# Kernel tuning notes

Hardware: AMD Instinct MI355X
Metric: run time of the kernel (lower is better)

## Reference

```python
import jax, jax.numpy as jnp
import numpy as np
from jax import lax


def _conv(x, w, b, pad, dil):
    # standard NCHW conv, OIHW weights
    y = lax.conv_general_dilated(x, w, (1, 1), [(pad, pad), (pad, pad)],
                                 rhs_dilation=(dil, dil),
                                 dimension_numbers=('NCHW', 'OIHW', 'NCHW'))
    return y + b[None, :, None, None]


def _bilinear(img, py, px):
    # img: [B,C,H,W]; py,px: [B,KK,H,W] float sample positions.
    # Zero-padding bilinear sampling (torchvision deform_conv semantics):
    # each of the 4 corners contributes 0 if it lies outside the image.
    B, C, H, W = img.shape
    y0 = jnp.floor(py)
    x0 = jnp.floor(px)
    wy1 = py - y0
    wx1 = px - x0
    imgf = img.reshape(B, C, H * W)

    def corner(yi, xi, wgt):
        valid = (yi >= 0) & (yi <= H - 1) & (xi >= 0) & (xi <= W - 1)
        yc = jnp.clip(yi, 0, H - 1).astype(jnp.int32)
        xc = jnp.clip(xi, 0, W - 1).astype(jnp.int32)
        idx = yc * W + xc  # [B,KK,H,W]
        g = jax.vmap(lambda im, ix: jnp.take(im, ix.reshape(-1), axis=1))(imgf, idx)
        g = g.reshape(B, C, *yi.shape[1:])  # [B,C,KK,H,W]
        return g * (wgt * valid.astype(img.dtype))[:, None]

    return (corner(y0, x0, (1 - wy1) * (1 - wx1))
            + corner(y0, x0 + 1, (1 - wy1) * wx1)
            + corner(y0 + 1, x0, wy1 * (1 - wx1))
            + corner(y0 + 1, x0 + 1, wy1 * wx1))


def _deform_dw(x, off_w, off_b, dw_w, K, pad, dil):
    # offset-predicted deformable depthwise conv (groups == channels)
    B, C, H, W = x.shape
    off = _conv(x, off_w, off_b, pad, dil).reshape(B, K * K, 2, H, W)
    dy, dx = off[:, :, 0], off[:, :, 1]  # torchvision order: (dy, dx) per tap
    ky, kx = jnp.meshgrid(jnp.arange(K), jnp.arange(K), indexing='ij')
    by = (ky.reshape(-1) * dil - pad).astype(x.dtype)  # [KK]
    bx = (kx.reshape(-1) * dil - pad).astype(x.dtype)
    py = jnp.arange(H, dtype=x.dtype)[None, None, :, None] + by[None, :, None, None] + dy
    px = jnp.arange(W, dtype=x.dtype)[None, None, None, :] + bx[None, :, None, None] + dx
    s = _bilinear(x, py, px)  # [B,C,KK,H,W]
    return jnp.einsum('bckhw,ck->bchw', s, dw_w.reshape(C, K * K))


def setup_inputs() -> dict:
    key = jax.random.key(0)
    ks = jax.random.split(key, 9)
    B, C, H, W = 4, 64, 56, 56
    f = lambda k, shape, s: jax.random.normal(k, shape, jnp.float32) * s
    return dict(
        x=f(ks[0], (B, C, H, W), 1.0),
        off_w1=f(ks[1], (2 * 5 * 5, C, 5, 5), 0.01), off_b1=f(ks[2], (2 * 5 * 5,), 0.01),
        dw_w1=f(ks[3], (C, 1, 5, 5), 0.1),
        off_w2=f(ks[4], (2 * 7 * 7, C, 7, 7), 0.01), off_b2=f(ks[5], (2 * 7 * 7,), 0.01),
        dw_w2=f(ks[6], (C, 1, 7, 7), 0.1),
        pw_w=f(ks[7], (C, C, 1, 1), 0.05), pw_b=f(ks[8], (C,), 0.05),
    )


def reference(x, off_w1, off_b1, dw_w1, off_w2, off_b2, dw_w2, pw_w, pw_b):
    attn = _deform_dw(x, off_w1, off_b1, dw_w1, 5, 2, 1)       # 5x5 deformable dw
    attn = _deform_dw(attn, off_w2, off_b2, dw_w2, 7, 9, 3)    # 7x7 dil-3 deformable dw
    attn = _conv(attn, pw_w, pw_b, 0, 1)                       # 1x1 pointwise
    return x * attn                                            # gated multiply
```

## Files before the change

kernel.cpp:

```cpp
#include <hip/hip_runtime.h>

#define BB 4
#define CC 64
#define HH 56
#define WW 56
#define HW (HH*WW)

typedef unsigned short u16;
typedef unsigned int u32;
typedef __attribute__((ext_vector_type(8))) short bf16x8;
typedef __attribute__((ext_vector_type(4))) float f32x4;

__device__ __forceinline__ u16 f2bf(float f) {
    union { float f; unsigned u; } c; c.f = f;
    unsigned u = c.u;
    u = (u + 0x7FFFu + ((u >> 16) & 1u)) >> 16;
    return (u16)u;
}
__device__ __forceinline__ float lo_f(u32 u) {
    union { unsigned u; float f; } c; c.u = u << 16; return c.f;
}
__device__ __forceinline__ float hi_f(u32 u) {
    union { unsigned u; float f; } c; c.u = u & 0xffff0000u; return c.f;
}

#define R1 102400
#define R2 401408
#define R3 4096
#define R4 1600
#define R5 3136
#define TGRID (BB*(HW/64))
#define PREPN (R1+R2+R3+R4+R5)
__global__ __launch_bounds__(256)
void prep_tr_kernel(const float* __restrict__ x,
                    const float* __restrict__ ow1, const float* __restrict__ ow2,
                    const float* __restrict__ pw,  const float* __restrict__ dw1,
                    const float* __restrict__ dw2,
                    u16* __restrict__ xT,
                    u16* __restrict__ w2t1, u16* __restrict__ w2t2,
                    u16* __restrict__ pwT, float* __restrict__ dwT1,
                    float* __restrict__ dwT2) {
    __shared__ u16 tile[64][72];
    const int t = threadIdx.x;
    if (blockIdx.x < TGRID) {
        const int blk = blockIdx.x;
        const int b   = blk / (HW/64);
        const int p0  = (blk % (HW/64))*64;
        const int px  = t & 63, icq = t >> 6;
        const float* ip = x + ((size_t)b*CC + icq*16)*HW + p0 + px;
        #pragma unroll
        for (int i = 0; i < 16; ++i)
            tile[px][icq*16 + i] = f2bf(ip[(size_t)i*HW]);
        __syncthreads();
        const int px2 = t >> 2, g = t & 3;
        u16* op = xT + ((size_t)b*HW + p0 + px2)*64 + g*16;
        const uint4* s = (const uint4*)&tile[px2][g*16];
        ((uint4*)op)[0] = s[0];
        ((uint4*)op)[1] = s[1];
        return;
    }
    const int i = (blockIdx.x - TGRID)*256 + t;
    if (i < R1) {
        const int ic = i & 63, n = (i >> 6) & 63, tap = i >> 12;
        w2t1[i] = f2bf((n < 50) ? ow1[((size_t)n*64 + ic)*25 + tap] : 0.f);
    } else if (i < R1+R2) {
        const int j = i - R1;
        const int ic = j & 63, n = (j >> 6) & 127, tap = j >> 13;
        w2t2[j] = f2bf((n < 98) ? ow2[((size_t)n*64 + ic)*49 + tap] : 0.f);
    } else if (i < R1+R2+R3) {
        const int j = i - (R1+R2);
        pwT[j] = f2bf(pw[j]);
    } else if (i < R1+R2+R3+R4) {
        const int j = i - (R1+R2+R3);
        const int c = j & 63, k = j >> 6;
        dwT1[j] = dw1[c*25 + k];
    } else if (i < R1+R2+R3+R4+R5) {
        const int j = i - (R1+R2+R3+R4);
        const int c = j & 63, k = j >> 6;
        dwT2[j] = dw2[c*49 + k];
    }
}

__device__ __forceinline__ uint4 selz(bool v, uint4 a) {
    const uint4 z = make_uint4(0,0,0,0);
    return v ? a : z;
}

template<int K, int DIL, int PAD, int COUT, int NP, int NPAD, int NTW>
__global__ __launch_bounds__(256, 4)
void conv_mfma_lds_kernel(const u16* __restrict__ xT, const u16* __restrict__ w2t,
                          const float* __restrict__ bias, float* __restrict__ out) {
    constexpr int KK = K*K;
    constexpr int BROWS = 16*NTW;
    __shared__ u16 Ab[2][64*64];
    __shared__ u16 Bb[2][BROWS*64];

    const int nm   = HW/64;
    const int b    = blockIdx.x / nm;
    const int p0   = (blockIdx.x % nm)*64;
    const int nt0  = blockIdx.y;
    const int t    = threadIdx.x;
    const int wave = t >> 6;
    const int lane = t & 63;

    const int spx = t >> 3;
    const int sc  = t & 7;
    const int pA  = p0 + spx;
    const int pB  = p0 + spx + 32;
    const int pyA = pA / WW, pxA = pA % WW;
    const int pyB = pB / WW, pxB = pB % WW;
    const u16* xb = xT + (size_t)b*HW*64;
    const int sslotA = ((sc + spx) & 7)*8;
    const int bn  = t >> 3;
    const int bslot = ((sc + bn) & 7)*8;
    const u16* wbase = w2t + (size_t)nt0*BROWS*64;

    const int r = lane & 15, quad = lane >> 4;
    const int mloc = wave*16 + r;
    const int arow = mloc*64;
    const int a0s = ((quad     + mloc) & 7)*8;
    const int a1s = ((quad + 4 + mloc) & 7)*8;
    const int b0s = ((quad     + r) & 7)*8;
    const int b1s = ((quad + 4 + r) & 7)*8;

    f32x4 acc[NTW];
    #pragma unroll
    for (int h = 0; h < NTW; ++h) acc[h] = (f32x4){0.f,0.f,0.f,0.f};
    const uint4 z4 = make_uint4(0,0,0,0);

    auto LD = [&](int tap, uint4& a0, uint4& a1, bool& va, bool& vb, uint4& bb) {
        const int dyy = (tap/K)*DIL - PAD;
        const int dxx = (tap%K)*DIL - PAD;
        const int off = dyy*WW + dxx;
        {
            const int yy = pyA + dyy, xx = pxA + dxx;
            va = ((unsigned)yy < (unsigned)HH) && ((unsigned)xx < (unsigned)WW);
            a0 = *(const uint4*)(xb + (size_t)(va ? (pA + off) : 0)*64 + sc*8);
        }
        {
            const int yy = pyB + dyy, xx = pxB + dxx;
            vb = ((unsigned)yy < (unsigned)HH) && ((unsigned)xx < (unsigned)WW);
            a1 = *(const uint4*)(xb + (size_t)(vb ? (pB + off) : 0)*64 + sc*8);
        }
        if (BROWS == 32 || bn < BROWS)
            bb = *(const uint4*)(wbase + ((size_t)tap*NP + bn)*64 + sc*8);
    };

    uint4 rA0 = z4, rA1 = z4, rB = z4;
    bool v0 = false, v1 = false;
    LD(0, rA0, rA1, v0, v1, rB);

    #pragma unroll
    for (int tap = 0; tap < KK; ++tap) {
        uint4 nA0 = z4, nA1 = z4, nB = z4;
        bool nv0 = false, nv1 = false;
        if (tap + 1 < KK) LD(tap + 1, nA0, nA1, nv0, nv1, nB);

        u16* A  = &Ab[tap & 1][0];
        u16* Bq = &Bb[tap & 1][0];
        *(uint4*)(A + spx*64      + sslotA) = selz(v0, rA0);
        *(uint4*)(A + (spx+32)*64 + sslotA) = selz(v1, rA1);
        if (BROWS == 32 || bn < BROWS) *(uint4*)(Bq + bn*64 + bslot) = rB;
        __syncthreads();

        const bf16x8 av0 = *(const bf16x8*)(A + arow + a0s);
        const bf16x8 av1 = *(const bf16x8*)(A + arow + a1s);
        #pragma unroll
        for (int h = 0; h < NTW; ++h) {
            const int brow = (h*16 + r)*64;
            const bf16x8 bv0 = *(const bf16x8*)(Bq + brow + b0s);
            const bf16x8 bv1 = *(const bf16x8*)(Bq + brow + b1s);
            acc[h] = __builtin_amdgcn_mfma_f32_16x16x32_bf16(av0, bv0, acc[h], 0, 0, 0);
            acc[h] = __builtin_amdgcn_mfma_f32_16x16x32_bf16(av1, bv1, acc[h], 0, 0, 0);
        }

        rA0 = nA0; rA1 = nA1; rB = nB; v0 = nv0; v1 = nv1;
    }

    #pragma unroll
    for (int h = 0; h < NTW; ++h) {
        const int n = nt0*BROWS + h*16 + r;
        if (n < COUT) {
            const float bv = bias[n];
            float* op = out + ((size_t)b*HW + p0 + wave*16 + quad*4)*NPAD + n;
            #pragma unroll
            for (int r2 = 0; r2 < 4; ++r2) op[(size_t)r2*NPAD] = acc[h][r2] + bv;
        }
    }
}

template<int K, int DIL, int PAD, int NPAD>
__global__ __launch_bounds__(256)
void deform_cl_kernel(const u16* __restrict__ inT, const float* __restrict__ offT,
                      const float* __restrict__ dwT, u16* __restrict__ outT) {
    constexpr int KK = K*K;
    __shared__ float4 swt[8][KK];
    __shared__ int4   sat[8][KK];
    __shared__ float  sdw[KK*64];

    const int t = threadIdx.x;
    const int nb8 = (BB*HW/8) >> 3;
    const int blk0 = blockIdx.x;
    const int blk = (blk0 & 7)*nb8 + (blk0 >> 3);
    const int p0 = blk*8;
    const int b  = p0 / HW;
    const int pl0 = p0 - b*HW;

    for (int i = t; i < KK*64; i += 256) sdw[i] = dwT[i];

    for (int i = t; i < 8*KK; i += 256) {
        const int pix = i / KK, k = i - pix*KK;
        const int pl  = pl0 + pix;
        const int h = pl / WW, w = pl % WW;
        const float* orow = offT + ((size_t)b*HW + pl)*NPAD;
        const float dy = orow[2*k];
        const float dx = orow[2*k+1];
        const float py = (float)(h + (k/K)*DIL - PAD) + dy;
        const float px = (float)(w + (k%K)*DIL - PAD) + dx;
        const float y0f = floorf(py), x0f = floorf(px);
        const float wy1 = py - y0f,  wx1 = px - x0f;
        const float wy0 = 1.f - wy1, wx0 = 1.f - wx1;
        const int y0 = (int)y0f, x0 = (int)x0f;

        const int y0c = min(max(y0,   0), HH-1);
        const int y1c = min(max(y0+1, 0), HH-1);
        const int x0c = min(max(x0,   0), WW-1);
        const int x1c = min(max(x0+1, 0), WW-1);
        const float gy0 = wy0 * ((y0   >= 0 && y0   < HH) ? 1.f : 0.f);
        const float gy1 = wy1 * ((y0+1 >= 0 && y0+1 < HH) ? 1.f : 0.f);
        const float gx0 = wx0 * ((x0   >= 0 && x0   < WW) ? 1.f : 0.f);
        const float gx1 = wx1 * ((x0+1 >= 0 && x0+1 < WW) ? 1.f : 0.f);

        swt[pix][k] = make_float4(gy0*gx0, gy0*gx1, gy1*gx0, gy1*gx1);
        const int r0 = y0c*WW, r1 = y1c*WW;
        sat[pix][k] = make_int4((r0 + x0c) << 7, (r0 + x1c) << 7,
                                (r1 + x0c) << 7, (r1 + x1c) << 7);
    }
    __syncthreads();

    const int wave = t >> 6, lane = t & 63;
    const int pixl = 2*wave + (lane >> 5);
    const int chp  = lane & 31;
    const char* ib = (const char*)(inT + (size_t)b*HW*64) + chp*4;

    float accx = 0.f, accy = 0.f;

    int4   av[4];
    float4 wv[2];
    float2 dv[2];
    u32 c00[3], c01[3], c10[3], c11[3];

    av[0] = sat[pixl][0];
    if (KK > 1) av[1] = sat[pixl][1];
    if (KK > 2) av[2] = sat[pixl][2];
    wv[0] = swt[pixl][0];
    dv[0] = *(const float2*)&sdw[2*chp];
    c00[0] = *(const u32*)(ib + av[0].x);
    c01[0] = *(const u32*)(ib + av[0].y);
    c10[0] = *(const u32*)(ib + av[0].z);
    c11[0] = *(const u32*)(ib + av[0].w);
    if (KK > 1) {
        c00[1] = *(const u32*)(ib + av[1].x);
        c01[1] = *(const u32*)(ib + av[1].y);
        c10[1] = *(const u32*)(ib + av[1].z);
        c11[1] = *(const u32*)(ib + av[1].w);
    }

    #pragma unroll
    for (int k = 0; k < KK; ++k) {
        if (k + 3 < KK) av[(k+3)&3] = sat[pixl][k+3];
        if (k + 2 < KK) {
            const int4 a = av[(k+2)&3];
            c00[(k+2)%3] = *(const u32*)(ib + a.x);
            c01[(k+2)%3] = *(const u32*)(ib + a.y);
            c10[(k+2)%3] = *(const u32*)(ib + a.z);
            c11[(k+2)%3] = *(const u32*)(ib + a.w);
        }
        if (k + 1 < KK) {
            wv[(k+1)&1] = swt[pixl][k+1];
            dv[(k+1)&1] = *(const float2*)&sdw[(k+1)*64 + 2*chp];
        }
        const float4 w = wv[k&1];
        const u32 u00 = c00[k%3], u01 = c01[k%3], u10 = c10[k%3], u11 = c11[k%3];
        const float sx = lo_f(u00)*w.x + lo_f(u01)*w.y + lo_f(u10)*w.z + lo_f(u11)*w.w;
        const float sy = hi_f(u00)*w.x + hi_f(u01)*w.y + hi_f(u10)*w.z + hi_f(u11)*w.w;
        const float2 d = dv[k&1];
        accx += sx * d.x;
        accy += sy * d.y;
    }

    const u32 o = (u32)f2bf(accx) | ((u32)f2bf(accy) << 16);
    *(u32*)((char*)outT + (size_t)(p0 + pixl)*128 + chp*4) = o;
}

__global__ __launch_bounds__(256)
void pw_mfma_kernel(const u16* __restrict__ a2T, const u16* __restrict__ pwT,
                    const float* __restrict__ pb, const float* __restrict__ x,
                    float* __restrict__ out) {
    const int nm = HW/64;
    const int b  = blockIdx.x / nm;
    const int p0 = (blockIdx.x % nm)*64 + (threadIdx.x >> 6)*16;
    const int nt = blockIdx.y;
    const int lane = threadIdx.x & 63;
    const int r = lane & 15, quad = lane >> 4;

    const u16* ap = a2T + ((size_t)b*HW + p0 + r)*64 + quad*8;
    f32x4 acc = (f32x4){0.f,0.f,0.f,0.f};
    #pragma unroll
    for (int ks = 0; ks < 2; ++ks) {
        const bf16x8 av = *(const bf16x8*)(ap + ks*32);
        const bf16x8 bv = *(const bf16x8*)(pwT + ((size_t)(nt*16 + r))*64 + ks*32 + quad*8);
        acc = __builtin_amdgcn_mfma_f32_16x16x32_bf16(av, bv, acc, 0, 0, 0);
    }

    const int n = nt*16 + r;
    const float bv = pb[n];
    const size_t base = ((size_t)b*CC + n)*HW + p0 + quad*4;
    #pragma unroll
    for (int r2 = 0; r2 < 4; ++r2)
        out[base + r2] = x[base + r2] * (acc[r2] + bv);
}

template<int K, int DIL, int PAD, int COUT, int OCB>
__global__ __launch_bounds__(256)
void off_conv_sg_kernel(const float* __restrict__ in, const float* __restrict__ wgt,
                        const float* __restrict__ bias, float* __restrict__ out) {
    constexpr int KK = K*K;
    const int nOB = COUT / OCB;
    const int b   = blockIdx.x / nOB;
    const int oc0 = (blockIdx.x % nOB) * OCB;
    const int x   = threadIdx.x;
    const int h   = blockIdx.y*4 + threadIdx.y;

    float acc[OCB];
    #pragma unroll
    for (int o = 0; o < OCB; ++o) acc[o] = bias[oc0+o];

    const float* inb = in + (size_t)b*CC*HW;
    const float* wb  = wgt + (size_t)oc0*CC*KK;

    for (int ic = 0; ic < CC; ++ic) {
        const float* inp = inb + ic*HW;
        const float* wp  = wb + ic*KK;
        #pragma unroll
        for (int ky = 0; ky < K; ++ky) {
            const int  y  = h + ky*DIL - PAD;
            const bool yv = (y >= 0) && (y < HH);
            const int  yc = yv ? y : 0;
            const float* row = inp + yc*WW;
            #pragma unroll
            for (int kx = 0; kx < K; ++kx) {
                const int  xx = x + kx*DIL - PAD;
                const bool v  = yv && (xx >= 0) && (xx < WW);
                const int  xc = (xx < 0) ? 0 : ((xx >= WW) ? (WW-1) : xx);
                float val = row[xc];
                val = v ? val : 0.f;
                const int t = ky*K + kx;
                #pragma unroll
                for (int o = 0; o < OCB; ++o)
                    acc[o] += wp[(size_t)o*CC*KK + t] * val;
            }
        }
    }

    if (x >= WW) return;
    #pragma unroll
    for (int o = 0; o < OCB; ++o)
        out[((size_t)b*COUT + oc0 + o)*HW + h*WW + x] = acc[o];
}

template<int K, int DIL, int PAD>
__global__ __launch_bounds__(64)
void deform_dw_full_kernel(const float* __restrict__ in, const float* __restrict__ off,
                           const float* __restrict__ dw, float* __restrict__ out) {
    constexpr int KK = K*K;
    const int idx = blockIdx.x*64 + threadIdx.x;
    const int x = idx % WW;
    const int h = (idx / WW) % HH;
    const int c = (idx / HW) % CC;
    const int b = idx / (CC*HW);

    const float* inp  = in  + ((size_t)b*CC + c)*HW;
    const float* offp = off + (size_t)b*(2*KK)*HW + h*WW + x;
    const float* dwp  = dw  + c*KK;

    float acc = 0.f;
    #pragma unroll 7
    for (int k = 0; k < KK; ++k) {
        const float dy = offp[(2*k  )*HW];
        const float dx = offp[(2*k+1)*HW];
        const float py = (float)(h + (k/K)*DIL - PAD) + dy;
        const float px = (float)(x + (k%K)*DIL - PAD) + dx;
        const float y0f = floorf(py), x0f = floorf(px);
        const float wy1 = py - y0f,  wx1 = px - x0f;
        const float wy0 = 1.f - wy1, wx0 = 1.f - wx1;
        const int y0 = (int)y0f, x0 = (int)x0f;

        const int y0c = min(max(y0,   0), HH-1);
        const int y1c = min(max(y0+1, 0), HH-1);
        const int x0c = min(max(x0,   0), WW-1);
        const int x1c = min(max(x0+1, 0), WW-1);
        const float my0 = (y0   >= 0 && y0   < HH) ? 1.f : 0.f;
        const float my1 = (y0+1 >= 0 && y0+1 < HH) ? 1.f : 0.f;
        const float mx0 = (x0   >= 0 && x0   < WW) ? 1.f : 0.f;
        const float mx1 = (x0+1 >= 0 && x0+1 < WW) ? 1.f : 0.f;

        const float v00 = inp[y0c*WW + x0c];
        const float v01 = inp[y0c*WW + x1c];
        const float v10 = inp[y1c*WW + x0c];
        const float v11 = inp[y1c*WW + x1c];

        const float gx0 = wx0*mx0, gx1 = wx1*mx1;
        const float s = (v00*gx0 + v01*gx1) * (wy0*my0)
                      + (v10*gx0 + v11*gx1) * (wy1*my1);
        acc += s * dwp[k];
    }
    out[idx] = acc;
}

__global__ __launch_bounds__(256)
void pw_mul_kernel(const float* __restrict__ x, const float* __restrict__ a2,
                   const float* __restrict__ pw, const float* __restrict__ pb,
                   float* __restrict__ out) {
    constexpr int HW4 = HW/4;
    const int t = blockIdx.x*256 + threadIdx.x;
    if (t >= BB*CC*HW4) return;
    const int sp4 = t % HW4;
    const int oc  = (t / HW4) % CC;
    const int b   = t / (CC*HW4);

    const float4* ap = (const float4*)(a2 + (size_t)b*CC*HW) + sp4;
    const float4* wp4 = (const float4*)(pw + oc*CC);
    const float pbv = pb[oc];
    float4 acc = make_float4(pbv, pbv, pbv, pbv);
    #pragma unroll 4
    for (int ic4 = 0; ic4 < CC/4; ++ic4) {
        const float4 w = wp4[ic4];
        float4 a0 = ap[(ic4*4+0)*HW4];
        float4 a1 = ap[(ic4*4+1)*HW4];
        float4 a2v = ap[(ic4*4+2)*HW4];
        float4 a3 = ap[(ic4*4+3)*HW4];
        acc.x += w.x*a0.x + w.y*a1.x + w.z*a2v.x + w.w*a3.x;
        acc.y += w.x*a0.y + w.y*a1.y + w.z*a2v.y + w.w*a3.y;
        acc.z += w.x*a0.z + w.y*a1.z + w.z*a2v.z + w.w*a3.z;
        acc.w += w.x*a0.w + w.y*a1.w + w.z*a2v.w + w.w*a3.w;
    }
    const float4 xv = ((const float4*)x)[t];
    float4 r;
    r.x = xv.x*acc.x; r.y = xv.y*acc.y; r.z = xv.z*acc.z; r.w = xv.w*acc.w;
    ((float4*)out)[t] = r;
}

extern "C" void kernel_launch(void* const* d_in, const int* in_sizes, int n_in,
                              void* d_out, int out_size, void* d_ws, size_t ws_size,
                              hipStream_t stream) {
    const float* x      = (const float*)d_in[0];
    const float* off_w1 = (const float*)d_in[1];
    const float* off_b1 = (const float*)d_in[2];
    const float* dw_w1  = (const float*)d_in[3];
    const float* off_w2 = (const float*)d_in[4];
    const float* off_b2 = (const float*)d_in[5];
    const float* dw_w2  = (const float*)d_in[6];
    const float* pw_w   = (const float*)d_in[7];
    const float* pw_b   = (const float*)d_in[8];
    float* out = (float*)d_out;

    const size_t nF    = (size_t)BB*CC*HW;
    const size_t attnB = nF*sizeof(float);
    const size_t off2B = (size_t)BB*98*HW*sizeof(float);
    const size_t offTB = (size_t)BB*HW*112*sizeof(float);
    const size_t chB   = (size_t)BB*HW*64*sizeof(u16);
    char* ws = (char*)d_ws;

    const int n    = (int)nF;
    const int dbl  = n/64;
    const int pbl  = (n/4 + 255)/256;
    dim3 cblk(64,4);
    dim3 rgrd1(BB*(50/5), HH/4);
    dim3 rgrd2(BB*(98/7), HH/4);
    dim3 cgrd1(TGRID, 2);
    dim3 cgrd2(TGRID, 4);
    dim3 pgrd(TGRID, 4);
    const int dgrid = BB*HW/8;

    const size_t oOFF  = 0;
    const size_t oXT   = oOFF + offTB;
    const size_t oA1T  = oXT  + chB;
    const size_t oA2T  = oA1T + chB;
    const size_t oW1   = oA2T + chB;
    const size_t oW2   = oW1  + (size_t)R1*2;
    const size_t oPWT  = oW2  + (size_t)R2*2;
    const size_t oDW1  = oPWT + (size_t)R3*2;
    const size_t oDW2  = oDW1 + (size_t)R4*4;
    const size_t TOT   = oDW2 + (size_t)R5*4;

    if (ws_size >= TOT) {
        float* off_buf = (float*)(ws + oOFF);
        u16*   xT      = (u16*)(ws + oXT);
        u16*   a1T     = (u16*)(ws + oA1T);
        u16*   a2T     = (u16*)(ws + oA2T);
        u16*   w2t1    = (u16*)(ws + oW1);
        u16*   w2t2    = (u16*)(ws + oW2);
        u16*   pwT     = (u16*)(ws + oPWT);
        float* dwT1    = (float*)(ws + oDW1);
        float* dwT2    = (float*)(ws + oDW2);

        prep_tr_kernel<<<TGRID + (PREPN+255)/256, 256, 0, stream>>>(
            x, off_w1, off_w2, pw_w, dw_w1, dw_w2,
            xT, w2t1, w2t2, pwT, dwT1, dwT2);

        conv_mfma_lds_kernel<5,1,2,50,64,64,2><<<cgrd1, 256, 0, stream>>>(xT, w2t1, off_b1, off_buf);
        deform_cl_kernel<5,1,2,64><<<dgrid, 256, 0, stream>>>(xT, off_buf, dwT1, a1T);

        conv_mfma_lds_kernel<7,3,9,98,128,112,2><<<cgrd2, 256, 0, stream>>>(a1T, w2t2, off_b2, off_buf);
        deform_cl_kernel<7,3,9,112><<<dgrid, 256, 0, stream>>>(a1T, off_buf, dwT2, a2T);

        pw_mfma_kernel<<<pgrd, 256, 0, stream>>>(a2T, pwT, pw_b, x, out);
    } else if (ws_size >= off2B + attnB) {
        float* off_buf = (float*)ws;
        float* attn1   = (float*)d_out;
        float* attn2   = (float*)(ws + off2B);
        off_conv_sg_kernel<5,1,2,50,5><<<rgrd1, cblk, 0, stream>>>(x, off_w1, off_b1, off_buf);
        deform_dw_full_kernel<5,1,2><<<dbl, 64, 0, stream>>>(x, off_buf, dw_w1, attn1);
        off_conv_sg_kernel<7,3,9,98,7><<<rgrd2, cblk, 0, stream>>>(attn1, off_w2, off_b2, off_buf);
        deform_dw_full_kernel<7,3,9><<<dbl, 64, 0, stream>>>(attn1, off_buf, dw_w2, attn2);
        pw_mul_kernel<<<pbl, 256, 0, stream>>>(x, attn2, pw_w, pw_b, out);
    } else {
        float* attn1 = (float*)d_out;
        float* attn2 = (float*)ws;
        float* off1  = (float*)ws;
        off_conv_sg_kernel<5,1,2,50,5><<<rgrd1, cblk, 0, stream>>>(x, off_w1, off_b1, off1);
        deform_dw_full_kernel<5,1,2><<<dbl, 64, 0, stream>>>(x, off1, dw_w1, attn1);
        float* off2 = (float*)(ws + attnB);
        off_conv_sg_kernel<7,3,9,98,7><<<rgrd2, cblk, 0, stream>>>(attn1, off_w2, off_b2, off2);
        deform_dw_full_kernel<7,3,9><<<dbl, 64, 0, stream>>>(attn1, off2, dw_w2, attn2);
        pw_mul_kernel<<<pbl, 256, 0, stream>>>(x, attn2, pw_w, pw_b, out);
    }
}
```

Measured before the change: 155.4 us.

## Fuse second deformable depthwise stage with pointwise MFMA and gating

Merges the 7x7 deformable depthwise kernel with the 1x1 pointwise conv and gated multiply. Each block computes 8 pixels of attention, stages the bf16 result in shared memory reused from the weight table, then runs MFMA against the pointwise weights and writes x*attn directly. This removes one launch and the a2T global write and read. In exchange the MFMA is only half used (16-row tile, 8 valid pixels), and the output stores are narrow and strided across channels.

Result: no change. 153.2 us (-1.5%).

```diff
diff --git a/kernel.cpp b/kernel.cpp
--- a/kernel.cpp
+++ b/kernel.cpp
@@ -293,32 +293,130 @@
     *(u32*)((char*)outT + (size_t)(p0 + pixl)*128 + chp*4) = o;
 }
 
+template<int K, int DIL, int PAD, int NPAD>
 __global__ __launch_bounds__(256)
-void pw_mfma_kernel(const u16* __restrict__ a2T, const u16* __restrict__ pwT,
-                    const float* __restrict__ pb, const float* __restrict__ x,
-                    float* __restrict__ out) {
-    const int nm = HW/64;
-    const int b  = blockIdx.x / nm;
-    const int p0 = (blockIdx.x % nm)*64 + (threadIdx.x >> 6)*16;
-    const int nt = blockIdx.y;
-    const int lane = threadIdx.x & 63;
+void deform_pw_kernel(const u16* __restrict__ inT, const float* __restrict__ offT,
+                      const float* __restrict__ dwT, const u16* __restrict__ pwT,
+                      const float* __restrict__ pb, const float* __restrict__ x,
+                      float* __restrict__ out) {
+    constexpr int KK = K*K;
+    __shared__ float4 swt[8][KK];
+    __shared__ int4   sat[8][KK];
+    __shared__ float  sdw[KK*64];
+
+    const int t = threadIdx.x;
+    const int nb8 = (BB*HW/8) >> 3;
+    const int blk0 = blockIdx.x;
+    const int blk = (blk0 & 7)*nb8 + (blk0 >> 3);
+    const int p0 = blk*8;
+    const int b  = p0 / HW;
+    const int pl0 = p0 - b*HW;
+
+    for (int i = t; i < KK*64; i += 256) sdw[i] = dwT[i];
+
+    for (int i = t; i < 8*KK; i += 256) {
+        const int pix = i / KK, k = i - pix*KK;
+        const int pl  = pl0 + pix;
+        const int h = pl / WW, w = pl % WW;
+        const float* orow = offT + ((size_t)b*HW + pl)*NPAD;
+        const float dy = orow[2*k];
+        const float dx = orow[2*k+1];
+        const float py = (float)(h + (k/K)*DIL - PAD) + dy;
+        const float px = (float)(w + (k%K)*DIL - PAD) + dx;
+        const float y0f = floorf(py), x0f = floorf(px);
+        const float wy1 = py - y0f,  wx1 = px - x0f;
+        const float wy0 = 1.f - wy1, wx0 = 1.f - wx1;
+        const int y0 = (int)y0f, x0 = (int)x0f;
+
+        const int y0c = min(max(y0,   0), HH-1);
+        const int y1c = min(max(y0+1, 0), HH-1);
+        const int x0c = min(max(x0,   0), WW-1);
+        const int x1c = min(max(x0+1, 0), WW-1);
+        const float gy0 = wy0 * ((y0   >= 0 && y0   < HH) ? 1.f : 0.f);
+        const float gy1 = wy1 * ((y0+1 >= 0 && y0+1 < HH) ? 1.f : 0.f);
+        const float gx0 = wx0 * ((x0   >= 0 && x0   < WW) ? 1.f : 0.f);
+        const float gx1 = wx1 * ((x0+1 >= 0 && x0+1 < WW) ? 1.f : 0.f);
+
+        swt[pix][k] = make_float4(gy0*gx0, gy0*gx1, gy1*gx0, gy1*gx1);
+        const int r0 = y0c*WW, r1 = y1c*WW;
+        sat[pix][k] = make_int4((r0 + x0c) << 7, (r0 + x1c) << 7,
+                                (r1 + x0c) << 7, (r1 + x1c) << 7);
+    }
+    __syncthreads();
+
+    const int wave = t >> 6, lane = t & 63;
+    const int pixl = 2*wave + (lane >> 5);
+    const int chp  = lane & 31;
+    const char* ib = (const char*)(inT + (size_t)b*HW*64) + chp*4;
+
+    float accx = 0.f, accy = 0.f;
+
+    int4   av[4];
+    float4 wv[2];
+    float2 dv[2];
+    u32 c00[3], c01[3], c10[3], c11[3];
+
+    av[0] = sat[pixl][0];
+    if (KK > 1) av[1] = sat[pixl][1];
+    if (KK > 2) av[2] = sat[pixl][2];
+    wv[0] = swt[pixl][0];
+    dv[0] = *(const float2*)&sdw[2*chp];
+    c00[0] = *(const u32*)(ib + av[0].x);
+    c01[0] = *(const u32*)(ib + av[0].y);
+    c10[0] = *(const u32*)(ib + av[0].z);
+    c11[0] = *(const u32*)(ib + av[0].w);
+    if (KK > 1) {
+        c00[1] = *(const u32*)(ib + av[1].x);
+        c01[1] = *(const u32*)(ib + av[1].y);
+        c10[1] = *(const u32*)(ib + av[1].z);
+        c11[1] = *(const u32*)(ib + av[1].w);
+    }
+
+    #pragma unroll
+    for (int k = 0; k < KK; ++k) {
+        if (k + 3 < KK) av[(k+3)&3] = sat[pixl][k+3];
+        if (k + 2 < KK) {
+            const int4 a = av[(k+2)&3];
+            c00[(k+2)%3] = *(const u32*)(ib + a.x);
+            c01[(k+2)%3] = *(const u32*)(ib + a.y);
+            c10[(k+2)%3] = *(const u32*)(ib + a.z);
+            c11[(k+2)%3] = *(const u32*)(ib + a.w);
+        }
+        if (k + 1 < KK) {
+            wv[(k+1)&1] = swt[pixl][k+1];
+            dv[(k+1)&1] = *(const float2*)&sdw[(k+1)*64 + 2*chp];
+        }
+        const float4 w = wv[k&1];
+        const u32 u00 = c00[k%3], u01 = c01[k%3], u10 = c10[k%3], u11 = c11[k%3];
+        const float sx = lo_f(u00)*w.x + lo_f(u01)*w.y + lo_f(u10)*w.z + lo_f(u11)*w.w;
+        const float sy = hi_f(u00)*w.x + hi_f(u01)*w.y + hi_f(u10)*w.z + hi_f(u11)*w.w;
+        const float2 d = dv[k&1];
+        accx += sx * d.x;
+        accy += sy * d.y;
+    }
+
+    __syncthreads();
+    u16* att = (u16*)&swt[0][0];
+    const u32 o = (u32)f2bf(accx) | ((u32)f2bf(accy) << 16);
+    *(u32*)((char*)att + pixl*128 + chp*4) = o;
+    __syncthreads();
+
     const int r = lane & 15, quad = lane >> 4;
-
-    const u16* ap = a2T + ((size_t)b*HW + p0 + r)*64 + quad*8;
-    f32x4 acc = (f32x4){0.f,0.f,0.f,0.f};
+    f32x4 pacc = (f32x4){0.f,0.f,0.f,0.f};
     #pragma unroll
     for (int ks = 0; ks < 2; ++ks) {
-        const bf16x8 av = *(const bf16x8*)(ap + ks*32);
-        const bf16x8 bv = *(const bf16x8*)(pwT + ((size_t)(nt*16 + r))*64 + ks*32 + quad*8);
-        acc = __builtin_amdgcn_mfma_f32_16x16x32_bf16(av, bv, acc, 0, 0, 0);
-    }
-
-    const int n = nt*16 + r;
-    const float bv = pb[n];
-    const size_t base = ((size_t)b*CC + n)*HW + p0 + quad*4;
-    #pragma unroll
-    for (int r2 = 0; r2 < 4; ++r2)
-        out[base + r2] = x[base + r2] * (acc[r2] + bv);
+        const bf16x8 pav = *(const bf16x8*)(att + r*64 + ks*32 + quad*8);
+        const bf16x8 pbv = *(const bf16x8*)(pwT + ((size_t)(wave*16 + r))*64 + ks*32 + quad*8);
+        pacc = __builtin_amdgcn_mfma_f32_16x16x32_bf16(pav, pbv, pacc, 0, 0, 0);
+    }
+    if (quad < 2) {
+        const int n = wave*16 + r;
+        const float bvb = pb[n];
+        const size_t base = ((size_t)b*CC + n)*HW + pl0 + quad*4;
+        #pragma unroll
+        for (int r2 = 0; r2 < 4; ++r2)
+            out[base + r2] = x[base + r2] * (pacc[r2] + bvb);
+    }
 }
 
 template<int K, int DIL, int PAD, int COUT, int OCB>
@@ -480,7 +578,6 @@
     dim3 rgrd2(BB*(98/7), HH/4);
     dim3 cgrd1(TGRID, 2);
     dim3 cgrd2(TGRID, 4);
-    dim3 pgrd(TGRID, 4);
     const int dgrid = BB*HW/8;
 
     const size_t oOFF  = 0;
@@ -498,7 +595,6 @@
         float* off_buf = (float*)(ws + oOFF);
         u16*   xT      = (u16*)(ws + oXT);
         u16*   a1T     = (u16*)(ws + oA1T);
-        u16*   a2T     = (u16*)(ws + oA2T);
         u16*   w2t1    = (u16*)(ws + oW1);
         u16*   w2t2    = (u16*)(ws + oW2);
         u16*   pwT     = (u16*)(ws + oPWT);
@@ -513,9 +609,7 @@
         deform_cl_kernel<5,1,2,64><<<dgrid, 256, 0, stream>>>(xT, off_buf, dwT1, a1T);
 
         conv_mfma_lds_kernel<7,3,9,98,128,112,2><<<cgrd2, 256, 0, stream>>>(a1T, w2t2, off_b2, off_buf);
-        deform_cl_kernel<7,3,9,112><<<dgrid, 256, 0, stream>>>(a1T, off_buf, dwT2, a2T);
-
-        pw_mfma_kernel<<<pgrd, 256, 0, stream>>>(a2T, pwT, pw_b, x, out);
+        deform_pw_kernel<7,3,9,112><<<dgrid, 256, 0, stream>>>(a1T, off_buf, dwT2, pwT, pw_b, x, out);
     } else if (ws_size >= off2B + attnB) {
         float* off_buf = (float*)ws;
         float* attn1   = (float*)d_out;
```
